# Performance work log

Measured on AMD Instinct MI355X. Metric: run time of the kernel, lower is better.

The kernel has to match this reference:

```python
import jax, jax.numpy as jnp
import numpy as np

D = 1024

def setup_inputs() -> dict:
    key = jax.random.key(0)
    ks = jax.random.split(key, 9)
    s = 1.0 / np.sqrt(D)
    x = jax.random.normal(ks[0], (4096, 8, D), dtype=jnp.float32)
    Wq = jax.random.uniform(ks[1], (D, D), jnp.float32, -s, s)
    bq = jax.random.uniform(ks[2], (D,), jnp.float32, -s, s)
    Wk = jax.random.uniform(ks[3], (D, D), jnp.float32, -s, s)
    bk = jax.random.uniform(ks[4], (D,), jnp.float32, -s, s)
    Wv = jax.random.uniform(ks[5], (D, D), jnp.float32, -s, s)
    bv = jax.random.uniform(ks[6], (D,), jnp.float32, -s, s)
    Wo = jax.random.uniform(ks[7], (D, D), jnp.float32, -s, s)
    bo = jax.random.uniform(ks[8], (D,), jnp.float32, -s, s)
    return {"x": x, "Wq": Wq, "bq": bq, "Wk": Wk, "bk": bk,
            "Wv": Wv, "bv": bv, "Wo": Wo, "bo": bo}

def reference(x, Wq, bq, Wk, bk, Wv, bv, Wo, bo):
    # x: (S, B, D) seq-first, matching torch module
    Q = jax.nn.elu(x @ Wq.T + bq) + 1.0  # (S,B,D)
    K = jax.nn.elu(x @ Wk.T + bk) + 1.0  # (S,B,D)
    V = x @ Wv.T + bv                    # (S,B,D)
    # KV = K^T V per batch: (B, D, D)
    KV = jnp.einsum('sbd,sbe->bde', K, V)
    # out = Q @ KV per batch, back to (S,B,D)
    out = jnp.einsum('sbd,bde->sbe', Q, KV)
    return out @ Wo.T + bo
```

## Files before the change

### kernel.cpp

```cpp
#include <hip/hip_runtime.h>


typedef __bf16 bf16;
typedef __attribute__((ext_vector_type(8))) __bf16 bf16x8;
typedef __attribute__((ext_vector_type(4))) __bf16 bf16x4;
typedef __attribute__((ext_vector_type(4))) float f32x4;

static constexpr int S = 4096;
static constexpr int B = 8;
static constexpr int D = 1024;
static constexpr int SB = S * B;
static constexpr long long NELEM = (long long)SB * D;

__device__ __forceinline__ void load_lds16(const bf16* g, void* l)
{
    __builtin_amdgcn_global_load_lds(
        (const __attribute__((address_space(1))) void*)g,
        (__attribute__((address_space(3))) void*)l, 16, 0, 0);
}

__global__ void cvt_f32_to_bf16(const float* __restrict__ in, bf16* __restrict__ out, int n)
{
    int i = (blockIdx.x * blockDim.x + threadIdx.x) * 4;
    int stride = gridDim.x * blockDim.x * 4;
    for (; i < n; i += stride) {
        float4 v = *(const float4*)(in + i);
        bf16x4 o;
        o[0] = (bf16)v.x; o[1] = (bf16)v.y; o[2] = (bf16)v.z; o[3] = (bf16)v.w;
        *(bf16x4*)(out + i) = o;
    }
}

__global__ __launch_bounds__(256) void cvt_transpose_1024(
    const float* __restrict__ in, bf16* __restrict__ out)
{
    __shared__ bf16 tile[64][72];
    const int e0 = blockIdx.y * 64;
    const int d0 = blockIdx.x * 64;
    const int t  = threadIdx.x;
    const int rl = t >> 3;
    const int c8 = (t & 7) * 8;
    #pragma unroll
    for (int p = 0; p < 2; ++p) {
        int r = rl + p * 32;
        float4 v0 = *(const float4*)(in + (long long)(e0 + r) * D + d0 + c8);
        float4 v1 = *(const float4*)(in + (long long)(e0 + r) * D + d0 + c8 + 4);
        tile[c8+0][r] = (bf16)v0.x; tile[c8+1][r] = (bf16)v0.y;
        tile[c8+2][r] = (bf16)v0.z; tile[c8+3][r] = (bf16)v0.w;
        tile[c8+4][r] = (bf16)v1.x; tile[c8+5][r] = (bf16)v1.y;
        tile[c8+6][r] = (bf16)v1.z; tile[c8+7][r] = (bf16)v1.w;
    }
    __syncthreads();
    #pragma unroll
    for (int p = 0; p < 2; ++p) {
        int dr = rl + p * 32;
        *(bf16x8*)(out + (long long)(d0 + dr) * D + e0 + c8) = *(bf16x8*)(&tile[dr][c8]);
    }
}

__global__ __launch_bounds__(256) void bvo_kernel(
    const float* __restrict__ Wo, const float* __restrict__ bv, float* __restrict__ bvo)
{
    const int row = blockIdx.x;
    const int t = threadIdx.x;
    float4 w = *(const float4*)(Wo + (long long)row * D + t * 4);
    float4 b = *(const float4*)(bv + t * 4);
    float s = w.x*b.x + w.y*b.y + w.z*b.z + w.w*b.w;
    __shared__ float red[256];
    red[t] = s; __syncthreads();
    for (int off = 128; off > 0; off >>= 1) {
        if (t < off) red[t] += red[t + off];
        __syncthreads();
    }
    if (t == 0) bvo[row] = red[0];
}

__global__ __launch_bounds__(256) void kv_add(const bf16* __restrict__ p, bf16* __restrict__ o)
{
    const long long DD = (long long)D * D;
    const int b = blockIdx.y;
    const long long i = ((long long)blockIdx.x * 256 + threadIdx.x) * 8;
    bf16x8 u = *(const bf16x8*)(p + (2 * b) * DD + i);
    bf16x8 v = *(const bf16x8*)(p + (2 * b + 1) * DD + i);
    bf16x8 r;
    #pragma unroll
    for (int j = 0; j < 8; ++j) r[j] = (bf16)((float)u[j] + (float)v[j]);
    *(bf16x8*)(o + b * DD + i) = r;
}

template<int BM, int BN, int WM, int WN, int EPI, int OUTF32, int BIASROW>
__global__ __launch_bounds__(WM * WN * 64, 2) void gemm_bt(
    const bf16* __restrict__ A, const bf16* __restrict__ Bm,
    const float* __restrict__ bias, void* __restrict__ Cout,
    int lda, int ldb, int ldc, int K,
    long long aBatch, long long bBatch, long long cBatch)
{
    constexpr int THREADS = WM * WN * 64;
    constexpr int WROWS = BM / WM, WCOLS = BN / WN;
    constexpr int MI = WROWS / 16, NI = WCOLS / 16;
    constexpr int ABYTES = BM * 64;
    constexpr int BBYTES = BN * 64;
    constexpr int BUF = ABYTES + BBYTES;

    __shared__ unsigned char smem[4 * BUF];

    const int tid  = threadIdx.x;
    const int lane = tid & 63;
    const int wave = tid >> 6;
    const int wr   = wave / WN;
    const int wc   = wave % WN;
    const int bz   = blockIdx.z;

    const int nx  = gridDim.x;
    const int bid = blockIdx.y * nx + blockIdx.x;
    const int cpx = (nx * gridDim.y) >> 3;
    const int swz = (bid & 7) * cpx + (bid >> 3);
    const long long m0 = (long long)(swz / nx) * BM;
    const long long n0 = (long long)(swz % nx) * BN;

    const bf16* Ab = A  + bz * aBatch + m0 * lda;
    const bf16* Bb = Bm + bz * bBatch + n0 * ldb;

    f32x4 acc[MI][NI] = {};
    const int NT = K >> 5;

    auto stage = [&](int t) {
        unsigned char* dst = smem + (t & 3) * BUF;
        const long long kk = (long long)t << 5;
        #pragma unroll
        for (int j = 0; j < 2; ++j) {
            const int g  = wave * 64 + lane + j * THREADS;
            const int gs = g ^ ((g >> 3) & 3);
            const int row = gs >> 2, col = (gs & 3) * 8;
            load_lds16(Ab + (long long)row * lda + kk + col,
                       dst + (wave * 64 + j * THREADS) * 16);
        }
        #pragma unroll
        for (int j = 0; j < 2; ++j) {
            const int g  = wave * 64 + lane + j * THREADS;
            const int gs = g ^ ((g >> 3) & 3);
            const int row = gs >> 2, col = (gs & 3) * 8;
            load_lds16(Bb + (long long)row * ldb + kk + col,
                       dst + ABYTES + (wave * 64 + j * THREADS) * 16);
        }
    };

    stage(0); stage(1); stage(2);

    const int ko2 = (lane >> 4) * 16;
    const int la15 = lane & 15;

    for (int t = 0; t < NT; ++t) {
        if (t + 2 < NT)      asm volatile("s_waitcnt vmcnt(8)" ::: "memory");
        else if (t + 1 < NT) asm volatile("s_waitcnt vmcnt(4)" ::: "memory");
        else                 asm volatile("s_waitcnt vmcnt(0)" ::: "memory");
        __builtin_amdgcn_s_barrier();
        asm volatile("" ::: "memory");

        if (t + 3 < NT) stage(t + 3);

        const unsigned char* buf = smem + (t & 3) * BUF;
        bf16x8 a[MI], b[NI];
        #pragma unroll
        for (int mi = 0; mi < MI; ++mi) {
            int ad = (wr * WROWS + mi * 16 + la15) * 64 + ko2;
            ad ^= ((ad >> 7) & 3) << 4;
            a[mi] = *(const bf16x8*)(buf + ad);
        }
        #pragma unroll
        for (int ni = 0; ni < NI; ++ni) {
            int ad = (wc * WCOLS + ni * 16 + la15) * 64 + ko2;
            ad ^= ((ad >> 7) & 3) << 4;
            b[ni] = *(const bf16x8*)(buf + ABYTES + ad);
        }

        __builtin_amdgcn_s_setprio(1);
        #pragma unroll
        for (int mi = 0; mi < MI; ++mi)
            #pragma unroll
            for (int ni = 0; ni < NI; ++ni)
                acc[mi][ni] = __builtin_amdgcn_mfma_f32_16x16x32_bf16(
                    a[mi], b[ni], acc[mi][ni], 0, 0, 0);
        __builtin_amdgcn_s_setprio(0);
    }

    const int crow = (lane >> 4) * 4;
    const int ccol = lane & 15;
    #pragma unroll
    for (int ni = 0; ni < NI; ++ni) {
        const long long c = n0 + wc * WCOLS + ni * 16 + ccol;
        float bcol = 0.0f;
        if (!BIASROW && bias) bcol = bias[c];
        #pragma unroll
        for (int mi = 0; mi < MI; ++mi) {
            const long long r0 = m0 + wr * WROWS + mi * 16 + crow;
            #pragma unroll
            for (int j = 0; j < 4; ++j) {
                float v = acc[mi][ni][j];
                v += BIASROW ? bias[r0 + j] : bcol;
                if (EPI == 1) v = (v > 0.0f) ? (v + 1.0f) : __expf(v);
                const long long idx = bz * cBatch + (r0 + j) * ldc + c;
                if (OUTF32) ((float*)Cout)[idx] = v;
                else        ((bf16*)Cout)[idx]  = (bf16)v;
            }
        }
    }
}

template<int EPI, int OUTF32, int BIASROW, int SPLITK>
__global__ __launch_bounds__(512, 1) void gemm8p(
    const bf16* __restrict__ A, const bf16* __restrict__ Bm,
    const float* __restrict__ bias, void* __restrict__ Cout,
    int lda, int ldb, int ldc, int K,
    long long aBatch, long long bBatch, long long cBatch)
{
    __shared__ unsigned char smem[131072];

    const int tid  = threadIdx.x;
    const int lane = tid & 63;
    const int wave = tid >> 6;
    const int wr   = wave >> 2;
    const int wc   = wave & 3;
    const int bz    = blockIdx.z;
    const int batch = bz / SPLITK;
    const int kseg  = bz % SPLITK;

    const int nx  = gridDim.x;
    const int bid = blockIdx.y * nx + blockIdx.x;
    const int cpx = (nx * gridDim.y) >> 3;
    const int swzb = (bid & 7) * cpx + (bid >> 3);
    const long long m0 = (long long)(swzb / nx) * 256;
    const long long n0 = (long long)(swzb % nx) * 256;

    const bf16* Ab = A  + batch * aBatch + m0 * lda + (long long)kseg * K;
    const bf16* Bb = Bm + batch * bBatch + n0 * ldb + (long long)kseg * K;

    const int sg = (lane & 3) ^ ((lane >> 3) & 3);
    const long long srow = wave * 32 + (lane >> 2);
    const bf16* srcA = Ab + srow * lda + sg * 8;
    const bf16* srcB = Bb + srow * ldb + sg * 8;
    const int dstoff = wave * 2048;

    const int la15 = lane & 15;
    const int rsw  = (lane >> 4) ^ ((la15 >> 1) & 3);
    const int a16  = (wr * 128 + la15) * 4 + rsw;
    const int b16  = (wc * 64  + la15) * 4 + rsw;

    f32x4 acc[8][4] = {};
    const int NT = K >> 6;
    const int NI = NT >> 1;

    auto stageA = [&](int T, int kh) {
        const int reg = ((((T & 1) << 1) | kh) << 14);
        const long long kp = ((long long)T << 6) + (kh << 5);
        load_lds16(srcA + kp,            smem + reg + dstoff);
        load_lds16(srcA + kp + 16 * lda, smem + reg + dstoff + 1024);
    };
    auto stageB = [&](int T, int kh) {
        const int reg = 65536 + ((((T & 1) << 1) | kh) << 14);
        const long long kp = ((long long)T << 6) + (kh << 5);
        load_lds16(srcB + kp,            smem + reg + dstoff);
        load_lds16(srcB + kp + 16 * ldb, smem + reg + dstoff + 1024);
    };

    stageB(0, 0); stageA(0, 0); stageB(0, 1); stageA(0, 1);
    stageB(1, 0); stageA(1, 0); stageB(1, 1);
    asm volatile("s_waitcnt vmcnt(10)" ::: "memory");
    __builtin_amdgcn_s_barrier();
    __builtin_amdgcn_sched_barrier(0);

    bf16x8 bfr[4];
    for (int i = 0; i < NI; ++i) {
        const int t = 2 * i;
        const bool nl = (i + 1 < NI);
        #pragma unroll
        for (int p = 0; p < 8; ++p) {
            const int ks  = (p >> 1) & 1;
            const int ch  = p & 1;
            const int buf = p >> 2;
            const int regA = ((buf << 1) | ks) << 14;
            const int regB = 65536 + regA;

            bf16x8 afr[4];
            if (ch == 0) {
                #pragma unroll
                for (int ni = 0; ni < 4; ++ni)
                    bfr[ni] = *(const bf16x8*)(smem + regB + (b16 + ni * 64) * 16);
            }
            #pragma unroll
            for (int m4 = 0; m4 < 4; ++m4)
                afr[m4] = *(const bf16x8*)(smem + regA + (a16 + (ch * 4 + m4) * 64) * 16);

            if      (p == 0) stageA(t + 1, 1);
            else if (p == 1) { if (t + 2 < NT) stageB(t + 2, 0); }
            else if (p == 2) { if (t + 2 < NT) stageA(t + 2, 0); }
            else if (p == 3) { if (t + 2 < NT) stageB(t + 2, 1); }
            else if (p == 4) { if (t + 2 < NT) stageA(t + 2, 1); }
            else if (p == 5) { if (t + 3 < NT) stageB(t + 3, 0); }
            else if (p == 6) { if (t + 3 < NT) stageA(t + 3, 0); }
            else             { if (t + 3 < NT) stageB(t + 3, 1); }

            if (p == 1) {
                if (nl) asm volatile("s_waitcnt vmcnt(6)" ::: "memory");
                else    asm volatile("s_waitcnt vmcnt(4)" ::: "memory");
            } else if (p == 5) {
                if (nl) asm volatile("s_waitcnt vmcnt(6)" ::: "memory");
                else    asm volatile("s_waitcnt vmcnt(0)" ::: "memory");
            }

            __builtin_amdgcn_s_barrier();
            asm volatile("s_waitcnt lgkmcnt(0)" ::: "memory");
            __builtin_amdgcn_s_setprio(1);
            #pragma unroll
            for (int m4 = 0; m4 < 4; ++m4)
                #pragma unroll
                for (int ni = 0; ni < 4; ++ni)
                    acc[ch * 4 + m4][ni] = __builtin_amdgcn_mfma_f32_16x16x32_bf16(
                        afr[m4], bfr[ni], acc[ch * 4 + m4][ni], 0, 0, 0);
            __builtin_amdgcn_s_setprio(0);
            __builtin_amdgcn_s_barrier();
            __builtin_amdgcn_sched_barrier(0);
        }
    }

    const bool doElu = (EPI == 1) || (EPI == 2 && m0 < 1024);
    const long long cb = (long long)bz * cBatch;
    const int crow = (lane >> 4) * 4;
    #pragma unroll
    for (int ni = 0; ni < 4; ++ni) {
        const long long c = n0 + wc * 64 + ni * 16 + la15;
        float bcol = 0.0f;
        if (!BIASROW && bias) bcol = bias[c];
        #pragma unroll
        for (int mi = 0; mi < 8; ++mi) {
            const long long r0 = m0 + wr * 128 + mi * 16 + crow;
            if (OUTF32) {
                float* p = (float*)Cout + cb + r0 * ldc + c;
                #pragma unroll
                for (int j = 0; j < 4; ++j) {
                    float v = acc[mi][ni][j] + (BIASROW ? bias[r0 + j] : bcol);
                    if (doElu) v = (v > 0.0f) ? (v + 1.0f) : __expf(v);
                    *p = v; p += ldc;
                }
            } else {
                bf16* p = (bf16*)Cout + cb + r0 * ldc + c;
                #pragma unroll
                for (int j = 0; j < 4; ++j) {
                    float v = acc[mi][ni][j] + (BIASROW ? bias[r0 + j] : bcol);
                    if (doElu) v = (v > 0.0f) ? (v + 1.0f) : __expf(v);
                    *p = (bf16)v; p += ldc;
                }
            }
        }
    }
}

extern "C" void kernel_launch(void* const* d_in, const int* in_sizes, int n_in,
                              void* d_out, int out_size, void* d_ws, size_t ws_size,
                              hipStream_t stream)
{
    const float* x  = (const float*)d_in[0];
    const float* Wq = (const float*)d_in[1];
    const float* bq = (const float*)d_in[2];
    const float* Wk = (const float*)d_in[3];
    const float* bk = (const float*)d_in[4];
    const float* Wv = (const float*)d_in[5];
    const float* bv = (const float*)d_in[6];
    const float* Wo = (const float*)d_in[7];
    const float* bo = (const float*)d_in[8];
    float* out = (float*)d_out;

    char* ws = (char*)d_ws;
    if (ws_size < (size_t)159383552) return;
    bf16*  xb   = (bf16*)(ws + 0);
    bf16*  part = (bf16*)(ws + 67108864);
    bf16*  Qb   = (bf16*)(ws + 67108864);
    bf16*  wvT  = (bf16*)(ws + 134217728);
    float* bkvo = (float*)(ws + 134217728 + 2097152);
    bf16*  KVo  = (bf16*)(ws + 134217728);
    bf16*  wqb  = (bf16*)(ws + 150994944);
    bf16*  wob  = wqb + 1048576;
    bf16*  wkvo = wob + 1048576;
    bf16*  KVb  = (bf16*)d_out;

    cvt_f32_to_bf16<<<4096, 256, 0, stream>>>(x,  xb,  (int)NELEM);
    cvt_f32_to_bf16<<<1024, 256, 0, stream>>>(Wq, wqb, D * D);
    cvt_f32_to_bf16<<<1024, 256, 0, stream>>>(Wo, wob, D * D);
    cvt_f32_to_bf16<<<1024, 256, 0, stream>>>(Wk, wkvo, D * D);
    cvt_transpose_1024<<<dim3(16, 16), 256, 0, stream>>>(Wv, wvT);
    bvo_kernel<<<1024, 256, 0, stream>>>(Wo, bv, bkvo + 1024);
    hipMemcpyAsync(bkvo, bk, D * sizeof(float), hipMemcpyDeviceToDevice, stream);

    gemm_bt<128, 128, 2, 2, 0, 0, 0><<<dim3(8, 8, 1), 256, 0, stream>>>(
        wob, wvT, nullptr, wkvo + (long long)1024 * 1024, D, D, D, D, 0, 0, 0);

    gemm8p<2, 0, 1, 1><<<dim3(16, 8, 8), 512, 0, stream>>>(
        wkvo, xb, bkvo, KVb, D, B * D, S, D,
        0, (long long)D, (long long)2048 * S);

    gemm8p<0, 0, 0, 2><<<dim3(4, 4, 16), 512, 0, stream>>>(
        KVb + (long long)1024 * S, KVb, nullptr, part, S, S, D, 2048,
        (long long)2048 * S, (long long)2048 * S, (long long)D * D);

    kv_add<<<dim3(512, 8), 256, 0, stream>>>(part, KVo);

    gemm8p<1, 0, 0, 1><<<dim3(4, 128, 1), 512, 0, stream>>>(
        xb, wqb, bq, Qb, D, D, D, D, 0, 0, 0);

    gemm8p<0, 1, 0, 1><<<dim3(4, 16, 8), 512, 0, stream>>>(
        Qb, KVo, bo, out, B * D, D, B * D, D,
        (long long)D, (long long)D * D, (long long)D);
}
```

Before: 538.0 us.

## Stage bf16 epilogue through LDS for coalesced stores and relax vmcnt waits

```diff
diff --git a/kernel.cpp b/kernel.cpp
--- a/kernel.cpp
+++ b/kernel.cpp
@@ -301,11 +301,16 @@
             else             { if (t + 3 < NT) stageB(t + 3, 1); }
 
             if (p == 1) {
-                if (nl) asm volatile("s_waitcnt vmcnt(6)" ::: "memory");
-                else    asm volatile("s_waitcnt vmcnt(4)" ::: "memory");
+                if (nl) asm volatile("s_waitcnt vmcnt(10)" ::: "memory");
+                else    asm volatile("s_waitcnt vmcnt(8)"  ::: "memory");
+            } else if (p == 3) {
+                if (nl) asm volatile("s_waitcnt vmcnt(10)" ::: "memory");
+                else    asm volatile("s_waitcnt vmcnt(4)"  ::: "memory");
             } else if (p == 5) {
-                if (nl) asm volatile("s_waitcnt vmcnt(6)" ::: "memory");
-                else    asm volatile("s_waitcnt vmcnt(0)" ::: "memory");
+                if (nl) asm volatile("s_waitcnt vmcnt(10)" ::: "memory");
+                else    asm volatile("s_waitcnt vmcnt(0)"  ::: "memory");
+            } else if (p == 7) {
+                if (nl) asm volatile("s_waitcnt vmcnt(10)" ::: "memory");
             }
 
             __builtin_amdgcn_s_barrier();
@@ -319,22 +324,22 @@
                         afr[m4], bfr[ni], acc[ch * 4 + m4][ni], 0, 0, 0);
             __builtin_amdgcn_s_setprio(0);
             __builtin_amdgcn_s_barrier();
-            __builtin_amdgcn_sched_barrier(0);
         }
     }
 
     const bool doElu = (EPI == 1) || (EPI == 2 && m0 < 1024);
     const long long cb = (long long)bz * cBatch;
     const int crow = (lane >> 4) * 4;
-    #pragma unroll
-    for (int ni = 0; ni < 4; ++ni) {
-        const long long c = n0 + wc * 64 + ni * 16 + la15;
-        float bcol = 0.0f;
-        if (!BIASROW && bias) bcol = bias[c];
-        #pragma unroll
-        for (int mi = 0; mi < 8; ++mi) {
-            const long long r0 = m0 + wr * 128 + mi * 16 + crow;
-            if (OUTF32) {
+
+    if constexpr (OUTF32 != 0) {
+        #pragma unroll
+        for (int ni = 0; ni < 4; ++ni) {
+            const long long c = n0 + wc * 64 + ni * 16 + la15;
+            float bcol = 0.0f;
+            if (!BIASROW && bias) bcol = bias[c];
+            #pragma unroll
+            for (int mi = 0; mi < 8; ++mi) {
+                const long long r0 = m0 + wr * 128 + mi * 16 + crow;
                 float* p = (float*)Cout + cb + r0 * ldc + c;
                 #pragma unroll
                 for (int j = 0; j < 4; ++j) {
@@ -342,14 +347,40 @@
                     if (doElu) v = (v > 0.0f) ? (v + 1.0f) : __expf(v);
                     *p = v; p += ldc;
                 }
-            } else {
-                bf16* p = (bf16*)Cout + cb + r0 * ldc + c;
+            }
+        }
+    } else {
+        bf16* lt = (bf16*)smem;
+        #pragma unroll
+        for (int half = 0; half < 2; ++half) {
+            __builtin_amdgcn_s_barrier();
+            if (wr == half) {
                 #pragma unroll
-                for (int j = 0; j < 4; ++j) {
-                    float v = acc[mi][ni][j] + (BIASROW ? bias[r0 + j] : bcol);
-                    if (doElu) v = (v > 0.0f) ? (v + 1.0f) : __expf(v);
-                    *p = (bf16)v; p += ldc;
+                for (int mi = 0; mi < 8; ++mi) {
+                    const int lrow = mi * 16 + crow;
+                    const long long r0 = m0 + half * 128 + lrow;
+                    #pragma unroll
+                    for (int ni = 0; ni < 4; ++ni) {
+                        const int lcol = wc * 64 + ni * 16 + la15;
+                        float bb = 0.0f;
+                        if (!BIASROW && bias) bb = bias[n0 + lcol];
+                        #pragma unroll
+                        for (int j = 0; j < 4; ++j) {
+                            float v = acc[mi][ni][j] + (BIASROW ? bias[r0 + j] : bb);
+                            if (doElu) v = (v > 0.0f) ? (v + 1.0f) : __expf(v);
+                            lt[(lrow + j) * 264 + lcol] = (bf16)v;
+                        }
+                    }
                 }
+            }
+            __builtin_amdgcn_s_barrier();
+            #pragma unroll
+            for (int it = 0; it < 8; ++it) {
+                const int chk = it * 512 + tid;
+                const int m   = chk >> 5;
+                const int nof = (chk & 31) * 8;
+                bf16x8 v = *(const bf16x8*)(lt + m * 264 + nof);
+                *(bf16x8*)((bf16*)Cout + cb + (m0 + half * 128 + m) * ldc + n0 + nof) = v;
             }
         }
     }
```

Result: faster. 527.4 us (-2.0%).
